# Performance work log

Hardware: AMD Instinct MI355X
Metric: run time of the kernel (lower is better)

Reference implementation:

```python
import jax, jax.numpy as jnp
import numpy as np

D_K = 64

def setup_inputs() -> dict:
    key = jax.random.key(0)
    ks = jax.random.split(key, 5)
    q = jax.random.normal(ks[0], (8, 4096, 64), dtype=jnp.float32)
    k = jax.random.normal(ks[1], (8, 4096, 64), dtype=jnp.float32)
    v = jax.random.normal(ks[2], (8, 4096, 64), dtype=jnp.float32)
    fc_w = jax.random.normal(ks[3], (64, 512), dtype=jnp.float32) * (1.0 / np.sqrt(64))
    fc_b = jnp.zeros((512,), dtype=jnp.float32)
    return {"q": q, "k": k, "v": v, "fc_w": fc_w, "fc_b": fc_b}

def reference(q, k, v, fc_w, fc_b):
    scale = 1.0 / jnp.sqrt(jnp.float32(D_K))
    # [B, Nq, Nk] score matrix
    attn = jnp.einsum('bqd,bkd->bqk', q, k) * scale
    attn = jax.nn.softmax(attn, axis=-1)
    out = jnp.einsum('bqk,bkd->bqd', attn, v)  # [B, Nq, d_v]
    return out @ fc_w + fc_b  # [B, Nq, d_model]
```

## Files before the change

kernel.cpp:

```cpp
#include <hip/hip_runtime.h>
#include <stdint.h>

#define BATCH  8
#define SEQ    4096
#define DK     64
#define DMODEL 512
#define QBLK   64
#define KBLK   64
#define NT     256

#define KWS_OFF   0u
#define VWS_OFF   4194304u
#define WWS_OFF   8388608u
#define WS_NEED   8454144u

typedef __attribute__((ext_vector_type(8))) short  short8;
typedef __attribute__((ext_vector_type(4))) float  f32x4;

__device__ __forceinline__ unsigned short f2bf(float x) {
  uint32_t u = __builtin_bit_cast(uint32_t, x);
  u += 0x7FFFu + ((u >> 16) & 1u);
  return (unsigned short)(u >> 16);
}
__device__ __forceinline__ uint32_t pack2(float a, float b) {
  return (uint32_t)f2bf(a) | ((uint32_t)f2bf(b) << 16);
}
__device__ __forceinline__ void async16(void* lds, const void* g) {
  __builtin_amdgcn_global_load_lds(
      (const __attribute__((address_space(1))) uint32_t*)g,
      (__attribute__((address_space(3))) uint32_t*)lds, 16, 0, 0);
}

__global__ __launch_bounds__(256)
void preconv(const float* __restrict__ kg_, const float* __restrict__ vg_,
             const float* __restrict__ wg_, unsigned char* __restrict__ ws) {
  int id = blockIdx.x * 256 + threadIdx.x;
  unsigned char* kws = ws + KWS_OFF;
  unsigned char* vws = ws + VWS_OFF;
  unsigned char* wws = ws + WWS_OFF;
  if (id < 262144) {
    int dg = id & 7, key = (id >> 3) & 63, t = (id >> 9) & 63, b = id >> 15;
    const float* src = kg_ + (((size_t)(b * 4096 + t * 64 + key)) << 6) + dg * 8;
    float4 a0 = *(const float4*)src;
    float4 a1 = *(const float4*)(src + 4);
    uint4 o;
    o.x = pack2(a0.x, a0.y); o.y = pack2(a0.z, a0.w);
    o.z = pack2(a1.x, a1.y); o.w = pack2(a1.z, a1.w);
    *(uint4*)(kws + (((size_t)(b * 64 + t)) << 13) +
              (uint32_t)(key * 128 + ((dg * 16) ^ ((key & 7) << 4)))) = o;
  } else if (id < 524288) {
    int iv = id - 262144;
    int kg2 = iv & 7, d = (iv >> 3) & 63, t = (iv >> 9) & 63, b = iv >> 15;
    const float* src = vg_ + (((size_t)(b * 4096 + t * 64 + kg2 * 8)) << 6) + d;
    float m[8];
    #pragma unroll
    for (int i = 0; i < 8; ++i) m[i] = src[i * 64];
    uint4 o;
    o.x = pack2(m[0], m[1]); o.y = pack2(m[2], m[3]);
    o.z = pack2(m[4], m[5]); o.w = pack2(m[6], m[7]);
    *(uint4*)(vws + (((size_t)(b * 64 + t)) << 13) +
              (uint32_t)(d * 128 + ((kg2 * 16) ^ ((d & 7) << 4)))) = o;
  } else if (id < 528384) {
    int iw = id - 524288;
    int kg2 = iw & 7, n = (iw >> 3) & 127, c = iw >> 10;
    const float* src = wg_ + (size_t)(kg2 * 8) * DMODEL + c * 128 + n;
    float m[8];
    #pragma unroll
    for (int i = 0; i < 8; ++i) m[i] = src[i * DMODEL];
    uint4 o;
    o.x = pack2(m[0], m[1]); o.y = pack2(m[2], m[3]);
    o.z = pack2(m[4], m[5]); o.w = pack2(m[6], m[7]);
    *(uint4*)(wws + c * 16384 + (uint32_t)(n * 128 + ((kg2 * 16) ^ ((n & 7) << 4)))) = o;
  }
}

struct SMemMain {
  unsigned char  kt[2][8192];
  unsigned char  vt[2][8192];
  unsigned short p[4][1024];
};
struct SMemEpi {
  unsigned char  wT[2][16384];
  unsigned short ob[4][1024];
};
union SMemU { SMemMain m; SMemEpi e; };
static_assert(sizeof(SMemU) == 40960, "LDS layout");

__global__ __launch_bounds__(NT, 2)
void attn_fc_fused2(const float* __restrict__ qg, const float* __restrict__ bg,
                    const unsigned char* __restrict__ ws, float* __restrict__ outg) {
  __shared__ SMemU sm;
  const int b    = blockIdx.x;
  const int qb   = blockIdx.y;
  const int tid  = threadIdx.x;
  const int wid  = tid >> 6;
  const int lane = tid & 63;
  const int l15  = lane & 15;
  const int g    = lane >> 4;
  const int g4   = g << 2;

  const unsigned char* kws = ws + KWS_OFF;
  const unsigned char* vws = ws + VWS_OFF;
  const unsigned char* wws = ws + WWS_OFF;
  const int    wb    = wid << 10;
  const int    ln16  = lane << 4;
  const size_t tbase = ((size_t)(b * 64)) << 13;

  const float SC = 0.125f * 1.44269504088896f;

  short8 qf[2];
  {
    const float* qp = qg + ((size_t)b * SEQ + (size_t)(qb * QBLK + wid * 16 + l15)) * DK + g * 8;
    #pragma unroll
    for (int ks2 = 0; ks2 < 2; ++ks2) {
      float4 a0 = *(const float4*)(qp + ks2 * 32);
      float4 a1 = *(const float4*)(qp + ks2 * 32 + 4);
      union { short8 v; uint32_t u[4]; } cv;
      cv.u[0] = pack2(a0.x * SC, a0.y * SC); cv.u[1] = pack2(a0.z * SC, a0.w * SC);
      cv.u[2] = pack2(a1.x * SC, a1.y * SC); cv.u[3] = pack2(a1.z * SC, a1.w * SC);
      qf[ks2] = cv.v;
    }
  }

  const f32x4 fz = {0.f, 0.f, 0.f, 0.f};
  f32x4 oacc[4];
  #pragma unroll
  for (int i = 0; i < 4; ++i) oacc[i] = fz;
  float lsum[4] = {0.f, 0.f, 0.f, 0.f};

  unsigned short* pbase = sm.m.p[wid];

#define STAGE_KV(buf, tt) do { \
    const unsigned char* ks_ = kws + tbase + (((size_t)(tt)) << 13); \
    const unsigned char* vs_ = vws + tbase + (((size_t)(tt)) << 13); \
    async16(sm.m.kt[buf] + wb,        ks_ + wb + ln16); \
    async16(sm.m.kt[buf] + wb + 4096, ks_ + wb + 4096 + ln16); \
    async16(sm.m.vt[buf] + wb,        vs_ + wb + ln16); \
    async16(sm.m.vt[buf] + wb + 4096, vs_ + wb + 4096 + ln16); \
  } while (0)

  STAGE_KV(0, 0);
  int cur = 0;
  #pragma unroll 1
  for (int t = 0; t < SEQ / KBLK; ++t) {
    __syncthreads();
    if (t + 1 < SEQ / KBLK) STAGE_KV(cur ^ 1, t + 1);

    const char* ktc = (const char*)sm.m.kt[cur];
    f32x4 s[4];
    #pragma unroll
    for (int t4 = 0; t4 < 4; ++t4) s[t4] = fz;
    #pragma unroll
    for (int ks2 = 0; ks2 < 2; ++ks2) {
      #pragma unroll
      for (int t4 = 0; t4 < 4; ++t4) {
        int key = l15 + t4 * 16;
        uint32_t off = (uint32_t)(key << 7) +
                       ((uint32_t)((g * 8 + ks2 * 32) << 1) ^ (uint32_t)((key & 7) << 4));
        short8 kf = *(const short8*)(ktc + off);
        s[t4] = __builtin_amdgcn_mfma_f32_16x16x32_bf16(qf[ks2], kf, s[t4], 0, 0, 0);
      }
    }

    #pragma unroll
    for (int t4 = 0; t4 < 4; ++t4)
      #pragma unroll
      for (int j = 0; j < 4; ++j) {
        float e = exp2f(s[t4][j]);
        s[t4][j] = e;
        lsum[j] += e;
      }

    #pragma unroll
    for (int t4 = 0; t4 < 4; ++t4)
      #pragma unroll
      for (int j = 0; j < 4; ++j) {
        int row = g4 + j;
        int col = l15 + t4 * 16;
        uint32_t off = (uint32_t)(row << 7) +
                       ((uint32_t)(col << 1) ^ (uint32_t)((row & 7) << 4));
        *(unsigned short*)((char*)pbase + off) = f2bf(s[t4][j]);
      }

    const char* vtc = (const char*)sm.m.vt[cur];
    #pragma unroll
    for (int ks2 = 0; ks2 < 2; ++ks2) {
      uint32_t aoff = (uint32_t)(l15 << 7) +
                      ((uint32_t)((g * 8 + ks2 * 32) << 1) ^ (uint32_t)((l15 & 7) << 4));
      short8 pa = *(const short8*)((const char*)pbase + aoff);
      #pragma unroll
      for (int dt = 0; dt < 4; ++dt) {
        int d = l15 + dt * 16;
        uint32_t boff = (uint32_t)(d << 7) +
                        ((uint32_t)((g * 8 + ks2 * 32) << 1) ^ (uint32_t)((d & 7) << 4));
        short8 vf = *(const short8*)(vtc + boff);
        oacc[dt] = __builtin_amdgcn_mfma_f32_16x16x32_bf16(pa, vf, oacc[dt], 0, 0, 0);
      }
    }
    cur ^= 1;
  }

  float inv[4];
  #pragma unroll
  for (int j = 0; j < 4; ++j) {
    float ts = lsum[j];
    #pragma unroll
    for (int off = 1; off < 16; off <<= 1) ts += __shfl_xor(ts, off, 64);
    inv[j] = 1.0f / ts;
  }
  unsigned short* obase = sm.e.ob[wid];
  #pragma unroll
  for (int dt = 0; dt < 4; ++dt)
    #pragma unroll
    for (int j = 0; j < 4; ++j) {
      int row = g4 + j;
      int col = l15 + dt * 16;
      uint32_t off = (uint32_t)(row << 7) +
                     ((uint32_t)(col << 1) ^ (uint32_t)((row & 7) << 4));
      *(unsigned short*)((char*)obase + off) = f2bf(oacc[dt][j] * inv[j]);
    }
  short8 af[2];
  #pragma unroll
  for (int ks2 = 0; ks2 < 2; ++ks2) {
    uint32_t off = (uint32_t)(l15 << 7) +
                   ((uint32_t)((g * 8 + ks2 * 32) << 1) ^ (uint32_t)((l15 & 7) << 4));
    af[ks2] = *(const short8*)((const char*)obase + off);
  }

#define STAGE_W(buf, cc) do { \
    const unsigned char* wsrc = wws + (uint32_t)(cc) * 16384u; \
    async16(sm.e.wT[buf] + wb,         wsrc + wb + ln16); \
    async16(sm.e.wT[buf] + wb + 4096,  wsrc + wb + 4096 + ln16); \
    async16(sm.e.wT[buf] + wb + 8192,  wsrc + wb + 8192 + ln16); \
    async16(sm.e.wT[buf] + wb + 12288, wsrc + wb + 12288 + ln16); \
  } while (0)

  __syncthreads();
  STAGE_W(0, 0);
  const int orow = qb * QBLK + wid * 16;
  #pragma unroll 1
  for (int c = 0; c < 4; ++c) {
    __syncthreads();
    if (c + 1 < 4) STAGE_W((c + 1) & 1, c + 1);
    const char* wtc = (const char*)sm.e.wT[c & 1];
    #pragma unroll
    for (int ntl = 0; ntl < 8; ++ntl) {
      int nl = l15 + ntl * 16;
      int n  = c * 128 + nl;
      f32x4 cacc = fz;
      #pragma unroll
      for (int ks2 = 0; ks2 < 2; ++ks2) {
        uint32_t off = (uint32_t)(nl << 7) +
                       ((uint32_t)((g * 8 + ks2 * 32) << 1) ^ (uint32_t)((nl & 7) << 4));
        short8 wf = *(const short8*)(wtc + off);
        cacc = __builtin_amdgcn_mfma_f32_16x16x32_bf16(af[ks2], wf, cacc, 0, 0, 0);
      }
      float bv = bg[n];
      #pragma unroll
      for (int j = 0; j < 4; ++j) {
        int qr = orow + g4 + j;
        outg[((size_t)b * SEQ + qr) * DMODEL + n] = cacc[j] + bv;
      }
    }
  }
}

struct F_SMemMain {
  unsigned short kt[KBLK * DK];
  unsigned short vt[DK * KBLK];
  unsigned short p[4][16 * KBLK];
};
struct F_SMemEpi {
  unsigned short wT[128 * DK];
  unsigned short ob[4][16 * DK];
};
union F_SMemU { F_SMemMain m; F_SMemEpi e; };

__global__ __launch_bounds__(NT, 2)
void attn_fc_fused_v1(const float* __restrict__ qg, const float* __restrict__ kg,
                      const float* __restrict__ vg, const float* __restrict__ wg,
                      const float* __restrict__ bg, float* __restrict__ outg) {
  __shared__ F_SMemU sm;
  const int b    = blockIdx.x;
  const int qb   = blockIdx.y;
  const int tid  = threadIdx.x;
  const int wid  = tid >> 6;
  const int lane = tid & 63;
  const int l15  = lane & 15;
  const int g    = lane >> 4;
  const int g4   = g << 2;

  short8 qf[2];
  {
    const float* qp = qg + ((size_t)b * SEQ + (size_t)(qb * QBLK + wid * 16 + l15)) * DK + g * 8;
    #pragma unroll
    for (int ks = 0; ks < 2; ++ks) {
      float4 a0 = *(const float4*)(qp + ks * 32);
      float4 a1 = *(const float4*)(qp + ks * 32 + 4);
      union { short8 v; uint32_t u[4]; } cv;
      cv.u[0] = pack2(a0.x, a0.y); cv.u[1] = pack2(a0.z, a0.w);
      cv.u[2] = pack2(a1.x, a1.y); cv.u[3] = pack2(a1.z, a1.w);
      qf[ks] = cv.v;
    }
  }
  const f32x4 fz = {0.f, 0.f, 0.f, 0.f};
  f32x4 oacc[4];
  #pragma unroll
  for (int i = 0; i < 4; ++i) oacc[i] = fz;
  float mrun[4], lrun[4];
  #pragma unroll
  for (int j = 0; j < 4; ++j) { mrun[j] = -1e30f; lrun[j] = 0.f; }
  const float SC = 0.125f * 1.44269504088896f;
  const float* kp0 = kg + (size_t)b * SEQ * DK;
  const float* vp0 = vg + (size_t)b * SEQ * DK;
  unsigned short* pbase = sm.m.p[wid];

  for (int t0 = 0; t0 < SEQ; t0 += KBLK) {
    __syncthreads();
    {
      const float* kp = kp0 + (size_t)t0 * DK;
      const float* vp = vp0 + (size_t)t0 * DK;
      #pragma unroll
      for (int r = 0; r < 4; ++r) {
        int f4  = r * 256 + tid;
        int key = f4 >> 4;
        int d0  = (f4 & 15) << 2;
        float4 kv = *(const float4*)(kp + f4 * 4);
        float4 vv = *(const float4*)(vp + f4 * 4);
        uint32_t koff = (uint32_t)(key << 7) +
                        ((uint32_t)(d0 << 1) ^ (uint32_t)((key & 7) << 4));
        *(uint2*)((char*)sm.m.kt + koff) = make_uint2(pack2(kv.x, kv.y), pack2(kv.z, kv.w));
        float vj[4] = {vv.x, vv.y, vv.z, vv.w};
        #pragma unroll
        for (int jj = 0; jj < 4; ++jj) {
          int d = d0 + jj;
          uint32_t voff = (uint32_t)(d << 7) +
                          ((uint32_t)(key << 1) ^ (uint32_t)((d & 7) << 4));
          *(unsigned short*)((char*)sm.m.vt + voff) = f2bf(vj[jj]);
        }
      }
    }
    __syncthreads();
    f32x4 s[4];
    #pragma unroll
    for (int t = 0; t < 4; ++t) s[t] = fz;
    #pragma unroll
    for (int ks = 0; ks < 2; ++ks) {
      #pragma unroll
      for (int t = 0; t < 4; ++t) {
        int key = l15 + t * 16;
        uint32_t off = (uint32_t)(key << 7) +
                       ((uint32_t)((g * 8 + ks * 32) << 1) ^ (uint32_t)((key & 7) << 4));
        short8 kf = *(const short8*)((const char*)sm.m.kt + off);
        s[t] = __builtin_amdgcn_mfma_f32_16x16x32_bf16(qf[ks], kf, s[t], 0, 0, 0);
      }
    }
    #pragma unroll
    for (int t = 0; t < 4; ++t)
      #pragma unroll
      for (int j = 0; j < 4; ++j) s[t][j] *= SC;
    float rsc[4], tsum[4];
    #pragma unroll
    for (int j = 0; j < 4; ++j) {
      float tm = fmaxf(fmaxf(s[0][j], s[1][j]), fmaxf(s[2][j], s[3][j]));
      #pragma unroll
      for (int off = 1; off < 16; off <<= 1) tm = fmaxf(tm, __shfl_xor(tm, off, 64));
      float nm = fmaxf(mrun[j], tm);
      rsc[j]  = exp2f(mrun[j] - nm);
      mrun[j] = nm;
      tsum[j] = 0.f;
    }
    #pragma unroll
    for (int t = 0; t < 4; ++t)
      #pragma unroll
      for (int j = 0; j < 4; ++j) {
        float e = exp2f(s[t][j] - mrun[j]);
        s[t][j] = e;
        tsum[j] += e;
      }
    #pragma unroll
    for (int j = 0; j < 4; ++j) {
      float ts = tsum[j];
      #pragma unroll
      for (int off = 1; off < 16; off <<= 1) ts += __shfl_xor(ts, off, 64);
      lrun[j] = lrun[j] * rsc[j] + ts;
    }
    #pragma unroll
    for (int dt = 0; dt < 4; ++dt)
      #pragma unroll
      for (int j = 0; j < 4; ++j) oacc[dt][j] *= rsc[j];
    #pragma unroll
    for (int t = 0; t < 4; ++t)
      #pragma unroll
      for (int j = 0; j < 4; ++j) {
        int row = g4 + j;
        int col = l15 + t * 16;
        uint32_t off = (uint32_t)(row << 7) +
                       ((uint32_t)(col << 1) ^ (uint32_t)((row & 7) << 4));
        *(unsigned short*)((char*)pbase + off) = f2bf(s[t][j]);
      }
    #pragma unroll
    for (int ks = 0; ks < 2; ++ks) {
      uint32_t aoff = (uint32_t)(l15 << 7) +
                      ((uint32_t)((g * 8 + ks * 32) << 1) ^ (uint32_t)((l15 & 7) << 4));
      short8 pa = *(const short8*)((const char*)pbase + aoff);
      #pragma unroll
      for (int dt = 0; dt < 4; ++dt) {
        int d = l15 + dt * 16;
        uint32_t boff = (uint32_t)(d << 7) +
                        ((uint32_t)((g * 8 + ks * 32) << 1) ^ (uint32_t)((d & 7) << 4));
        short8 vf = *(const short8*)((const char*)sm.m.vt + boff);
        oacc[dt] = __builtin_amdgcn_mfma_f32_16x16x32_bf16(pa, vf, oacc[dt], 0, 0, 0);
      }
    }
  }
  {
    float inv[4];
    #pragma unroll
    for (int j = 0; j < 4; ++j) inv[j] = 1.0f / lrun[j];
    unsigned short* obase = sm.e.ob[wid];
    #pragma unroll
    for (int dt = 0; dt < 4; ++dt)
      #pragma unroll
      for (int j = 0; j < 4; ++j) {
        int row = g4 + j;
        int col = l15 + dt * 16;
        uint32_t off = (uint32_t)(row << 7) +
                       ((uint32_t)(col << 1) ^ (uint32_t)((row & 7) << 4));
        *(unsigned short*)((char*)obase + off) = f2bf(oacc[dt][j] * inv[j]);
      }
    short8 af[2];
    #pragma unroll
    for (int ks = 0; ks < 2; ++ks) {
      uint32_t off = (uint32_t)(l15 << 7) +
                     ((uint32_t)((g * 8 + ks * 32) << 1) ^ (uint32_t)((l15 & 7) << 4));
      af[ks] = *(const short8*)((const char*)obase + off);
    }
    const int orow = qb * QBLK + wid * 16;
    #pragma unroll 1
    for (int nc = 0; nc < 4; ++nc) {
      __syncthreads();
      #pragma unroll
      for (int i = 0; i < 8; ++i) {
        int id = tid + i * 256;
        int n  = id & 127;
        int kk = (id >> 7) << 2;
        float w0 = wg[(kk + 0) * DMODEL + nc * 128 + n];
        float w1 = wg[(kk + 1) * DMODEL + nc * 128 + n];
        float w2 = wg[(kk + 2) * DMODEL + nc * 128 + n];
        float w3 = wg[(kk + 3) * DMODEL + nc * 128 + n];
        uint32_t off = (uint32_t)(n << 7) +
                       ((uint32_t)(kk << 1) ^ (uint32_t)((n & 7) << 4));
        *(uint2*)((char*)sm.e.wT + off) = make_uint2(pack2(w0, w1), pack2(w2, w3));
      }
      __syncthreads();
      #pragma unroll
      for (int ntl = 0; ntl < 8; ++ntl) {
        int nl = l15 + ntl * 16;
        int n  = nc * 128 + nl;
        f32x4 c = fz;
        #pragma unroll
        for (int ks = 0; ks < 2; ++ks) {
          uint32_t off = (uint32_t)(nl << 7) +
                         ((uint32_t)((g * 8 + ks * 32) << 1) ^ (uint32_t)((nl & 7) << 4));
          short8 wf = *(const short8*)((const char*)sm.e.wT + off);
          c = __builtin_amdgcn_mfma_f32_16x16x32_bf16(af[ks], wf, c, 0, 0, 0);
        }
        float bv = bg[n];
        #pragma unroll
        for (int j = 0; j < 4; ++j) {
          int qr = orow + g4 + j;
          outg[((size_t)b * SEQ + qr) * DMODEL + n] = c[j] + bv;
        }
      }
    }
  }
}

extern "C" void kernel_launch(void* const* d_in, const int* in_sizes, int n_in,
                              void* d_out, int out_size, void* d_ws, size_t ws_size,
                              hipStream_t stream) {
  (void)in_sizes; (void)n_in; (void)out_size;
  const float* q  = (const float*)d_in[0];
  const float* k  = (const float*)d_in[1];
  const float* v  = (const float*)d_in[2];
  const float* w  = (const float*)d_in[3];
  const float* bb = (const float*)d_in[4];
  float* out = (float*)d_out;
  if (ws_size >= WS_NEED && d_ws != nullptr) {
    preconv<<<dim3(2064), dim3(256), 0, stream>>>(k, v, w, (unsigned char*)d_ws);
    dim3 grid(BATCH, SEQ / QBLK);
    attn_fc_fused2<<<grid, dim3(NT), 0, stream>>>(q, bb, (const unsigned char*)d_ws, out);
  } else {
    dim3 grid(BATCH, SEQ / QBLK);
    attn_fc_fused_v1<<<grid, dim3(NT), 0, stream>>>(q, k, v, w, bb, out);
  }
}
```

Measured before the change: 96.37 us.

## Split attention over key halves with 32x32 MFMA and separate FC combine kernel

Replaces the fused attention+FC kernel with three steps. A split-K attention kernel uses 32x32x16 bf16 MFMA on 128-query blocks and two key halves, and keeps P in registers through permlane32 swaps instead of a round trip through LDS. A second kernel then combines the two partial outputs and row sums, normalizes, and applies the FC projection. This aims to raise MFMA efficiency and parallelism and to drop the P LDS traffic. In exchange it adds an extra launch and writes and reads fp32 partial outputs in global memory, and it only runs if the workspace is large enough.

```diff
diff --git a/kernel.cpp b/kernel.cpp
--- a/kernel.cpp
+++ b/kernel.cpp
@@ -1,4 +1,5 @@
 #include <hip/hip_runtime.h>
+#include <hip/hip_bf16.h>
 #include <stdint.h>
 
 #define BATCH  8
@@ -13,9 +14,13 @@
 #define VWS_OFF   4194304u
 #define WWS_OFF   8388608u
 #define WS_NEED   8454144u
-
-typedef __attribute__((ext_vector_type(8))) short  short8;
-typedef __attribute__((ext_vector_type(4))) float  f32x4;
+#define POFF      8454144u
+#define LOFF      (POFF + 16777216u)
+#define WS_NEED2  (LOFF + 262144u)
+
+typedef __attribute__((ext_vector_type(8)))  short short8;
+typedef __attribute__((ext_vector_type(4)))  float f32x4;
+typedef __attribute__((ext_vector_type(16))) float f32x16;
 
 __device__ __forceinline__ unsigned short f2bf(float x) {
   uint32_t u = __builtin_bit_cast(uint32_t, x);
@@ -24,6 +29,12 @@
 }
 __device__ __forceinline__ uint32_t pack2(float a, float b) {
   return (uint32_t)f2bf(a) | ((uint32_t)f2bf(b) << 16);
+}
+__device__ __forceinline__ uint32_t cvtpk2(float a, float b) {
+  __hip_bfloat162 h = __float22bfloat162_rn(make_float2(a, b));
+  uint32_t r;
+  __builtin_memcpy(&r, &h, 4);
+  return r;
 }
 __device__ __forceinline__ void async16(void* lds, const void* g) {
   __builtin_amdgcn_global_load_lds(
@@ -74,22 +85,152 @@
   }
 }
 
-struct SMemMain {
-  unsigned char  kt[2][8192];
-  unsigned char  vt[2][8192];
-  unsigned short p[4][1024];
-};
-struct SMemEpi {
+struct SMemA32 { unsigned char kt[2][8192]; unsigned char vt[2][8192]; };
+static_assert(sizeof(SMemA32) == 32768, "LDS layout");
+
+__global__ __launch_bounds__(NT, 2)
+void attn_split32(const float* __restrict__ qg, const unsigned char* __restrict__ ws,
+                  float* __restrict__ opart, float* __restrict__ lpart) {
+  __shared__ SMemA32 sm;
+  const int b    = blockIdx.x;
+  const int qb   = blockIdx.y;
+  const int z    = blockIdx.z;
+  const int tid  = threadIdx.x;
+  const int wid  = tid >> 6;
+  const int lane = tid & 63;
+  const int l31  = lane & 31;
+  const int hi   = lane >> 5;
+
+  const unsigned char* kws = ws + KWS_OFF;
+  const unsigned char* vws = ws + VWS_OFF;
+  const int    wstg  = wid << 11;
+  const int    ln16  = lane << 4;
+  const size_t tbase = ((size_t)(b * 64)) << 13;
+  const int    tt0   = z * 32;
+
+  const float SC = 0.125f * 1.44269504088896f;
+
+  const int qrow = qb * 128 + wid * 32 + l31;
+  short8 qf[4];
+  {
+    const float* qp = qg + ((size_t)b * SEQ + qrow) * DK;
+    #pragma unroll
+    for (int ds = 0; ds < 4; ++ds) {
+      const float* p = qp + ds * 16 + hi * 8;
+      float4 a0 = *(const float4*)p;
+      float4 a1 = *(const float4*)(p + 4);
+      union { short8 v; uint32_t u[4]; } cv;
+      cv.u[0] = cvtpk2(a0.x * SC, a0.y * SC); cv.u[1] = cvtpk2(a0.z * SC, a0.w * SC);
+      cv.u[2] = cvtpk2(a1.x * SC, a1.y * SC); cv.u[3] = cvtpk2(a1.z * SC, a1.w * SC);
+      qf[ds] = cv.v;
+    }
+  }
+
+  f32x16 o0, o1;
+  #pragma unroll
+  for (int r = 0; r < 16; ++r) { o0[r] = 0.f; o1[r] = 0.f; }
+  float lsum = 0.f;
+
+#define STG32(buf, tt) do { \
+    const unsigned char* ks_ = kws + tbase + (((size_t)(tt)) << 13); \
+    const unsigned char* vs_ = vws + tbase + (((size_t)(tt)) << 13); \
+    async16(sm.kt[buf] + wstg,        ks_ + wstg + ln16); \
+    async16(sm.kt[buf] + wstg + 1024, ks_ + wstg + 1024 + ln16); \
+    async16(sm.vt[buf] + wstg,        vs_ + wstg + ln16); \
+    async16(sm.vt[buf] + wstg + 1024, vs_ + wstg + 1024 + ln16); \
+  } while (0)
+
+  STG32(0, tt0);
+  int cur = 0;
+  #pragma unroll 1
+  for (int t = 0; t < 32; ++t) {
+    __syncthreads();
+    if (t + 1 < 32) STG32(cur ^ 1, tt0 + t + 1);
+
+    const char* ktc = (const char*)sm.kt[cur];
+    const char* vtc = (const char*)sm.vt[cur];
+
+    f32x16 s0, s1;
+    #pragma unroll
+    for (int r = 0; r < 16; ++r) { s0[r] = 0.f; s1[r] = 0.f; }
+    #pragma unroll
+    for (int ds = 0; ds < 4; ++ds) {
+      uint32_t cb   = (uint32_t)(ds * 32 + hi * 16);
+      uint32_t swz  = (uint32_t)((l31 & 7) << 4);
+      uint32_t off0 = ((uint32_t)l31 << 7)        + (cb ^ swz);
+      uint32_t off1 = ((uint32_t)(32 + l31) << 7) + (cb ^ swz);
+      short8 ka0 = *(const short8*)(ktc + off0);
+      short8 ka1 = *(const short8*)(ktc + off1);
+      s0 = __builtin_amdgcn_mfma_f32_32x32x16_bf16(ka0, qf[ds], s0, 0, 0, 0);
+      s1 = __builtin_amdgcn_mfma_f32_32x32x16_bf16(ka1, qf[ds], s1, 0, 0, 0);
+    }
+
+    #pragma unroll
+    for (int r = 0; r < 16; ++r) {
+      s0[r] = exp2f(s0[r]); lsum += s0[r];
+      s1[r] = exp2f(s1[r]); lsum += s1[r];
+    }
+
+    #pragma unroll
+    for (int ks = 0; ks < 4; ++ks) {
+      int ss = ks & 1;
+      uint32_t A0, A1, B0, B1;
+      if (ks < 2) {
+        A0 = cvtpk2(s0[8 * ss + 0], s0[8 * ss + 1]);
+        A1 = cvtpk2(s0[8 * ss + 2], s0[8 * ss + 3]);
+        B0 = cvtpk2(s0[8 * ss + 4], s0[8 * ss + 5]);
+        B1 = cvtpk2(s0[8 * ss + 6], s0[8 * ss + 7]);
+      } else {
+        A0 = cvtpk2(s1[8 * ss + 0], s1[8 * ss + 1]);
+        A1 = cvtpk2(s1[8 * ss + 2], s1[8 * ss + 3]);
+        B0 = cvtpk2(s1[8 * ss + 4], s1[8 * ss + 5]);
+        B1 = cvtpk2(s1[8 * ss + 6], s1[8 * ss + 7]);
+      }
+      asm("v_permlane32_swap_b32 %0, %1" : "+v"(A0), "+v"(B0));
+      asm("v_permlane32_swap_b32 %0, %1" : "+v"(A1), "+v"(B1));
+      union { short8 v; uint32_t u[4]; } pa;
+      pa.u[0] = A0; pa.u[1] = A1; pa.u[2] = B0; pa.u[3] = B1;
+
+      uint32_t kb = (uint32_t)(ks * 32 + hi * 16);
+      {
+        int d = l31;
+        uint32_t off = ((uint32_t)d << 7) + (kb ^ ((uint32_t)(d & 7) << 4));
+        short8 vf = *(const short8*)(vtc + off);
+        o0 = __builtin_amdgcn_mfma_f32_32x32x16_bf16(pa.v, vf, o0, 0, 0, 0);
+      }
+      {
+        int d = 32 + l31;
+        uint32_t off = ((uint32_t)d << 7) + (kb ^ ((uint32_t)(d & 7) << 4));
+        short8 vf = *(const short8*)(vtc + off);
+        o1 = __builtin_amdgcn_mfma_f32_32x32x16_bf16(pa.v, vf, o1, 0, 0, 0);
+      }
+    }
+    cur ^= 1;
+  }
+
+  float lt = lsum + __shfl_xor(lsum, 32, 64);
+  const size_t rbase = (size_t)(z * 8 + b) * 4096 + (size_t)(qb * 128 + wid * 32);
+  float* op = opart + rbase * 64;
+  #pragma unroll
+  for (int r = 0; r < 16; ++r) {
+    int qloc = (r & 3) + 8 * (r >> 2) + 4 * hi;
+    op[(size_t)qloc * 64 + l31]      = o0[r];
+    op[(size_t)qloc * 64 + 32 + l31] = o1[r];
+  }
+  if (hi == 0) lpart[rbase + l31] = lt;
+}
+
+struct SMemComb {
   unsigned char  wT[2][16384];
   unsigned short ob[4][1024];
 };
-union SMemU { SMemMain m; SMemEpi e; };
-static_assert(sizeof(SMemU) == 40960, "LDS layout");
+static_assert(sizeof(SMemComb) == 40960, "LDS layout");
 
 __global__ __launch_bounds__(NT, 2)
-void attn_fc_fused2(const float* __restrict__ qg, const float* __restrict__ bg,
-                    const unsigned char* __restrict__ ws, float* __restrict__ outg) {
-  __shared__ SMemU sm;
+void fc_combine(const float* __restrict__ opart, const float* __restrict__ lpart,
+                const unsigned char* __restrict__ ws, const float* __restrict__ bg,
+                float* __restrict__ outg) {
+  __shared__ SMemComb sm;
   const int b    = blockIdx.x;
   const int qb   = blockIdx.y;
   const int tid  = threadIdx.x;
@@ -99,125 +240,35 @@
   const int g    = lane >> 4;
   const int g4   = g << 2;
 
-  const unsigned char* kws = ws + KWS_OFF;
-  const unsigned char* vws = ws + VWS_OFF;
   const unsigned char* wws = ws + WWS_OFF;
-  const int    wb    = wid << 10;
-  const int    ln16  = lane << 4;
-  const size_t tbase = ((size_t)(b * 64)) << 13;
-
-  const float SC = 0.125f * 1.44269504088896f;
-
-  short8 qf[2];
-  {
-    const float* qp = qg + ((size_t)b * SEQ + (size_t)(qb * QBLK + wid * 16 + l15)) * DK + g * 8;
-    #pragma unroll
-    for (int ks2 = 0; ks2 < 2; ++ks2) {
-      float4 a0 = *(const float4*)(qp + ks2 * 32);
-      float4 a1 = *(const float4*)(qp + ks2 * 32 + 4);
-      union { short8 v; uint32_t u[4]; } cv;
-      cv.u[0] = pack2(a0.x * SC, a0.y * SC); cv.u[1] = pack2(a0.z * SC, a0.w * SC);
-      cv.u[2] = pack2(a1.x * SC, a1.y * SC); cv.u[3] = pack2(a1.z * SC, a1.w * SC);
-      qf[ks2] = cv.v;
-    }
-  }
+  const int wb   = wid << 10;
+  const int ln16 = lane << 4;
+
+  const float* op0 = opart + ((size_t)(0 * 8 + b) * 4096 + qb * 64) * 64;
+  const float* op1 = opart + ((size_t)(1 * 8 + b) * 4096 + qb * 64) * 64;
+  const float* l0  = lpart + (size_t)(0 * 8 + b) * 4096 + qb * 64;
+  const float* l1  = lpart + (size_t)(1 * 8 + b) * 4096 + qb * 64;
 
   const f32x4 fz = {0.f, 0.f, 0.f, 0.f};
-  f32x4 oacc[4];
-  #pragma unroll
-  for (int i = 0; i < 4; ++i) oacc[i] = fz;
-  float lsum[4] = {0.f, 0.f, 0.f, 0.f};
-
-  unsigned short* pbase = sm.m.p[wid];
-
-#define STAGE_KV(buf, tt) do { \
-    const unsigned char* ks_ = kws + tbase + (((size_t)(tt)) << 13); \
-    const unsigned char* vs_ = vws + tbase + (((size_t)(tt)) << 13); \
-    async16(sm.m.kt[buf] + wb,        ks_ + wb + ln16); \
-    async16(sm.m.kt[buf] + wb + 4096, ks_ + wb + 4096 + ln16); \
-    async16(sm.m.vt[buf] + wb,        vs_ + wb + ln16); \
-    async16(sm.m.vt[buf] + wb + 4096, vs_ + wb + 4096 + ln16); \
-  } while (0)
-
-  STAGE_KV(0, 0);
-  int cur = 0;
-  #pragma unroll 1
-  for (int t = 0; t < SEQ / KBLK; ++t) {
-    __syncthreads();
-    if (t + 1 < SEQ / KBLK) STAGE_KV(cur ^ 1, t + 1);
-
-    const char* ktc = (const char*)sm.m.kt[cur];
-    f32x4 s[4];
-    #pragma unroll
-    for (int t4 = 0; t4 < 4; ++t4) s[t4] = fz;
-    #pragma unroll
-    for (int ks2 = 0; ks2 < 2; ++ks2) {
-      #pragma unroll
-      for (int t4 = 0; t4 < 4; ++t4) {
-        int key = l15 + t4 * 16;
-        uint32_t off = (uint32_t)(key << 7) +
-                       ((uint32_t)((g * 8 + ks2 * 32) << 1) ^ (uint32_t)((key & 7) << 4));
-        short8 kf = *(const short8*)(ktc + off);
-        s[t4] = __builtin_amdgcn_mfma_f32_16x16x32_bf16(qf[ks2], kf, s[t4], 0, 0, 0);
-      }
-    }
-
-    #pragma unroll
-    for (int t4 = 0; t4 < 4; ++t4)
-      #pragma unroll
-      for (int j = 0; j < 4; ++j) {
-        float e = exp2f(s[t4][j]);
-        s[t4][j] = e;
-        lsum[j] += e;
-      }
-
-    #pragma unroll
-    for (int t4 = 0; t4 < 4; ++t4)
-      #pragma unroll
-      for (int j = 0; j < 4; ++j) {
-        int row = g4 + j;
-        int col = l15 + t4 * 16;
-        uint32_t off = (uint32_t)(row << 7) +
-                       ((uint32_t)(col << 1) ^ (uint32_t)((row & 7) << 4));
-        *(unsigned short*)((char*)pbase + off) = f2bf(s[t4][j]);
-      }
-
-    const char* vtc = (const char*)sm.m.vt[cur];
-    #pragma unroll
-    for (int ks2 = 0; ks2 < 2; ++ks2) {
-      uint32_t aoff = (uint32_t)(l15 << 7) +
-                      ((uint32_t)((g * 8 + ks2 * 32) << 1) ^ (uint32_t)((l15 & 7) << 4));
-      short8 pa = *(const short8*)((const char*)pbase + aoff);
-      #pragma unroll
-      for (int dt = 0; dt < 4; ++dt) {
-        int d = l15 + dt * 16;
-        uint32_t boff = (uint32_t)(d << 7) +
-                        ((uint32_t)((g * 8 + ks2 * 32) << 1) ^ (uint32_t)((d & 7) << 4));
-        short8 vf = *(const short8*)(vtc + boff);
-        oacc[dt] = __builtin_amdgcn_mfma_f32_16x16x32_bf16(pa, vf, oacc[dt], 0, 0, 0);
-      }
-    }
-    cur ^= 1;
-  }
 
   float inv[4];
   #pragma unroll
   for (int j = 0; j < 4; ++j) {
-    float ts = lsum[j];
-    #pragma unroll
-    for (int off = 1; off < 16; off <<= 1) ts += __shfl_xor(ts, off, 64);
-    inv[j] = 1.0f / ts;
-  }
-  unsigned short* obase = sm.e.ob[wid];
+    int row = wid * 16 + g4 + j;
+    inv[j] = 1.0f / (l0[row] + l1[row]);
+  }
+  unsigned short* obase = sm.ob[wid];
   #pragma unroll
   for (int dt = 0; dt < 4; ++dt)
     #pragma unroll
     for (int j = 0; j < 4; ++j) {
-      int row = g4 + j;
-      int col = l15 + dt * 16;
-      uint32_t off = (uint32_t)(row << 7) +
-                     ((uint32_t)(col << 1) ^ (uint32_t)((row & 7) << 4));
-      *(unsigned short*)((char*)obase + off) = f2bf(oacc[dt][j] * inv[j]);
+      int row  = wid * 16 + g4 + j;
+      int col  = l15 + dt * 16;
+      float o  = (op0[row * 64 + col] + op1[row * 64 + col]) * inv[j];
+      int rloc = g4 + j;
+      uint32_t off = (uint32_t)(rloc << 7) +
+                     ((uint32_t)(col << 1) ^ (uint32_t)((rloc & 7) << 4));
+      *(unsigned short*)((char*)obase + off) = f2bf(o);
     }
   short8 af[2];
   #pragma unroll
@@ -229,20 +280,19 @@
 
 #define STAGE_W(buf, cc) do { \
     const unsigned char* wsrc = wws + (uint32_t)(cc) * 16384u; \
-    async16(sm.e.wT[buf] + wb,         wsrc + wb + ln16); \
-    async16(sm.e.wT[buf] + wb + 4096,  wsrc + wb + 4096 + ln16); \
-    async16(sm.e.wT[buf] + wb + 8192,  wsrc + wb + 8192 + ln16); \
-    async16(sm.e.wT[buf] + wb + 12288, wsrc + wb + 12288 + ln16); \
+    async16(sm.wT[buf] + wb,         wsrc + wb + ln16); \
+    async16(sm.wT[buf] + wb + 4096,  wsrc + wb + 4096 + ln16); \
+    async16(sm.wT[buf] + wb + 8192,  wsrc + wb + 8192 + ln16); \
+    async16(sm.wT[buf] + wb + 12288, wsrc + wb + 12288 + ln16); \
   } while (0)
 
-  __syncthreads();
   STAGE_W(0, 0);
   const int orow = qb * QBLK + wid * 16;
   #pragma unroll 1
   for (int c = 0; c < 4; ++c) {
     __syncthreads();
     if (c + 1 < 4) STAGE_W((c + 1) & 1, c + 1);
-    const char* wtc = (const char*)sm.e.wT[c & 1];
+    const char* wtc = (const char*)sm.wT[c & 1];
     #pragma unroll
     for (int ntl = 0; ntl < 8; ++ntl) {
       int nl = l15 + ntl * 16;
@@ -487,12 +537,14 @@
   const float* w  = (const float*)d_in[3];
   const float* bb = (const float*)d_in[4];
   float* out = (float*)d_out;
-  if (ws_size >= WS_NEED && d_ws != nullptr) {
-    preconv<<<dim3(2064), dim3(256), 0, stream>>>(k, v, w, (unsigned char*)d_ws);
-    dim3 grid(BATCH, SEQ / QBLK);
-    attn_fc_fused2<<<grid, dim3(NT), 0, stream>>>(q, bb, (const unsigned char*)d_ws, out);
+  unsigned char* ws = (unsigned char*)d_ws;
+  if (ws_size >= WS_NEED2 && d_ws != nullptr) {
+    preconv<<<dim3(2064), dim3(256), 0, stream>>>(k, v, w, ws);
+    attn_split32<<<dim3(BATCH, SEQ / 128, 2), dim3(NT), 0, stream>>>(
+        q, ws, (float*)(ws + POFF), (float*)(ws + LOFF));
+    fc_combine<<<dim3(BATCH, SEQ / QBLK), dim3(NT), 0, stream>>>(
+        (const float*)(ws + POFF), (const float*)(ws + LOFF), ws, bb, out);
   } else {
-    dim3 grid(BATCH, SEQ / QBLK);
-    attn_fc_fused_v1<<<grid, dim3(NT), 0, stream>>>(q, k, v, w, bb, out);
-  }
-}
+    attn_fc_fused_v1<<<dim3(BATCH, SEQ / QBLK), dim3(NT), 0, stream>>>(q, k, v, w, bb, out);
+  }
+}
```

Result: faster. 89.42 us (-7.2%).
